# Kernel optimization log

Hardware: AMD Instinct MI355X
Metric: run time of the kernel (lower is better)

## Reference

```python
import jax, jax.numpy as jnp
import numpy as np

DIM_CAP = 16   # capsule dim
NCLS = 17      # annotation_nr
BS = 16
T = 120        # chunk_size * fps
P = 22         # players per frame graph
G = BS * T     # number of graphs = 1920
N = G * P      # nodes = 42240
C_IN = 14
CHS = [16, 32, 64, 152]  # 8m,16m,32m,76m with m=2
BN_EPS = 1e-3


def _build_graph():
    # fully-connected directed edges within each 22-node graph (no self loops)
    ii, jj = np.meshgrid(np.arange(P), np.arange(P), indexing='ij')
    mask = ii != jj
    li, lj = ii[mask], jj[mask]               # (462,)
    base = (np.arange(G) * P)[:, None]
    src = (base + li[None, :]).reshape(-1)
    dst = (base + lj[None, :]).reshape(-1)
    edge_index = np.stack([src, dst]).astype(np.int64)   # (2, E)
    batch = np.repeat(np.arange(G), P).astype(np.int64)  # (N,)
    return jnp.asarray(edge_index), jnp.asarray(batch)


def setup_inputs() -> dict:
    key = jax.random.key(0)
    ks = jax.random.split(key, 16)
    edge_index, batch = _build_graph()
    E = edge_index.shape[1]
    x = jax.random.normal(ks[0], (N, C_IN), dtype=jnp.float32)
    edge_attr = jax.random.uniform(ks[1], (E, 5), dtype=jnp.float32)
    dims = [C_IN] + CHS
    params = {}
    for i in range(4):
        s = 1.0 / np.sqrt(dims[i])
        params[f'W{i+1}'] = jax.random.normal(ks[2 + i], (dims[i], dims[i + 1]), dtype=jnp.float32) * s
        params[f'b{i+1}'] = jnp.zeros((dims[i + 1],), dtype=jnp.float32)
    c_out = DIM_CAP * NCLS  # 272
    params['conv_w'] = jax.random.normal(ks[6], (c_out, CHS[-1], 3), dtype=jnp.float32) * (1.0 / np.sqrt(CHS[-1] * 3))
    params['conv_b'] = jnp.zeros((c_out,), dtype=jnp.float32)
    params['bn_gamma'] = jnp.ones((T,), dtype=jnp.float32)
    params['bn_beta'] = jnp.zeros((T,), dtype=jnp.float32)
    return dict(x=x, edge_index=edge_index, batch=batch, edge_attr=edge_attr, **params)


def _gcn_layer(x, src, dst, w_edge, W, b):
    # PyG GCNConv: x' = D^-1/2 (A + I) D^-1/2 (x W) + b, edge weights w, self-loop weight 1
    n = x.shape[0]
    h = x @ W
    loop = jnp.arange(n)
    src_f = jnp.concatenate([src, loop])
    dst_f = jnp.concatenate([dst, loop])
    w_f = jnp.concatenate([w_edge, jnp.ones((n,), h.dtype)])
    deg = jax.ops.segment_sum(w_f, dst_f, num_segments=n)
    dinv = jnp.where(deg > 0, jax.lax.rsqrt(deg), 0.0)
    norm = dinv[src_f] * w_f * dinv[dst_f]
    out = jax.ops.segment_sum(norm[:, None] * h[src_f], dst_f, num_segments=n)
    return out + b


def reference(x, edge_index, batch, edge_attr, W1, b1, W2, b2, W3, b3, W4, b4,
              conv_w, conv_b, bn_gamma, bn_beta):
    src, dst = edge_index[0], edge_index[1]
    ew = edge_attr[:, 4]
    h = jax.nn.relu(_gcn_layer(x, src, dst, ew, W1, b1))
    h = jax.nn.relu(_gcn_layer(h, src, dst, ew, W2, b2))
    h = jax.nn.relu(_gcn_layer(h, src, dst, ew, W3, b3))
    h = jax.nn.relu(_gcn_layer(h, src, dst, ew, W4, b4))
    # global mean pool per graph -> (G, 152)
    ones = jnp.ones((h.shape[0],), h.dtype)
    cnt = jax.ops.segment_sum(ones, batch, num_segments=G)
    pooled = jax.ops.segment_sum(h, batch, num_segments=G) / jnp.clip(cnt, 1.0)[:, None]
    # (BS, T, 152) -> (BS, 152, T); conv kernel (3,1) with pad (1,1) on T
    feat = pooled.reshape(BS, T, CHS[-1]).transpose(0, 2, 1)
    conv = jax.lax.conv_general_dilated(
        feat, conv_w, window_strides=(1,), padding=[(1, 1)],
        dimension_numbers=('NCH', 'OIH', 'NCH'))
    conv = conv + conv_b[None, :, None]            # (BS, 272, T)
    caps = conv.transpose(0, 2, 1).reshape(BS, T, DIM_CAP, NCLS)
    # BatchNorm2d(num_features=T) in eval mode: running mean 0, var 1
    scale = (bn_gamma / jnp.sqrt(1.0 + BN_EPS))[None, :, None, None]
    shift = bn_beta[None, :, None, None]
    s = jax.nn.sigmoid(caps * scale + shift)
    out = jnp.sqrt(jnp.sum(jnp.square(s - 0.5), axis=2) * 4.0 / DIM_CAP)
    return out  # (BS, T, NCLS)
```

## Files before the change

### kernel.cpp

```cpp
#include <hip/hip_runtime.h>

#define GROUPS 1920
#define CH4 152

__device__ __forceinline__ int rh(int r) { return (r + (r >> 3)) & 7; }
__device__ __forceinline__ int swz(int r, int c) {
    return (r << 5) + ((((c >> 2) ^ rh(r)) << 2) | (c & 3));
}
__device__ __forceinline__ int swz4(int r, int c4) {
    return (r << 5) + ((c4 ^ rh(r)) << 2);
}

template<int DIN, int KR>
__device__ __forceinline__ void layerA(const float* buf, float* Ut,
                                       const float* A, int tid)
{
    constexpr int NT = (DIN / KR) * 3;
    if (tid < NT) {
        const int kt = tid / 3, pt = tid - kt * 3;
        const int p0 = pt * 8;
        float acc[KR][8];
        #pragma unroll
        for (int j = 0; j < KR; ++j)
            #pragma unroll
            for (int a = 0; a < 8; ++a) acc[j][a] = 0.f;
        #pragma unroll 2
        for (int q = 0; q < 22; ++q) {
            const float4 a0 = *(const float4*)(A + q * 28 + p0);
            const float4 a1 = *(const float4*)(A + q * 28 + p0 + 4);
            float xv[KR];
            #pragma unroll
            for (int j = 0; j < KR; ++j) xv[j] = buf[swz(kt * KR + j, q)];
            #pragma unroll
            for (int j = 0; j < KR; ++j) {
                acc[j][0] = fmaf(xv[j], a0.x, acc[j][0]);
                acc[j][1] = fmaf(xv[j], a0.y, acc[j][1]);
                acc[j][2] = fmaf(xv[j], a0.z, acc[j][2]);
                acc[j][3] = fmaf(xv[j], a0.w, acc[j][3]);
                acc[j][4] = fmaf(xv[j], a1.x, acc[j][4]);
                acc[j][5] = fmaf(xv[j], a1.y, acc[j][5]);
                acc[j][6] = fmaf(xv[j], a1.z, acc[j][6]);
                acc[j][7] = fmaf(xv[j], a1.w, acc[j][7]);
            }
        }
        #pragma unroll
        for (int j = 0; j < KR; ++j) {
            const int k = kt * KR + j;
            *(float4*)(Ut + swz4(k, pt * 2)) =
                make_float4(acc[j][0], acc[j][1], acc[j][2], acc[j][3]);
            *(float4*)(Ut + swz4(k, pt * 2 + 1)) =
                make_float4(acc[j][4], acc[j][5], acc[j][6], acc[j][7]);
        }
    }
}

template<int DIN, int DOUT, int CR>
__device__ __forceinline__ void layerB(const float* __restrict__ W,
                                       const float* __restrict__ Bb,
                                       const float* Ut, float* buf, int tid)
{
    constexpr int NT = (DOUT / CR) * 3;
    if (tid < NT) {
        const int ct = tid / 3, pt = tid - ct * 3;
        const int c0 = ct * CR;
        float acc[CR][8];
        #pragma unroll
        for (int b = 0; b < CR; ++b) {
            const float bias = Bb[c0 + b];
            #pragma unroll
            for (int a = 0; a < 8; ++a) acc[b][a] = bias;
        }
        #pragma unroll 4
        for (int k = 0; k < DIN; ++k) {
            const float4 u0 = *(const float4*)(Ut + swz4(k, pt * 2));
            const float4 u1 = *(const float4*)(Ut + swz4(k, pt * 2 + 1));
            float wv[CR];
            if constexpr (CR == 1) {
                wv[0] = W[k * DOUT + c0];
            } else if constexpr (CR == 2) {
                const float2 w2 = *(const float2*)(W + k * DOUT + c0);
                wv[0] = w2.x; wv[1] = w2.y;
            } else {
                #pragma unroll
                for (int b = 0; b < CR; b += 4) {
                    const float4 w4 = *(const float4*)(W + k * DOUT + c0 + b);
                    wv[b] = w4.x; wv[b + 1] = w4.y; wv[b + 2] = w4.z; wv[b + 3] = w4.w;
                }
            }
            #pragma unroll
            for (int b = 0; b < CR; ++b) {
                acc[b][0] = fmaf(wv[b], u0.x, acc[b][0]);
                acc[b][1] = fmaf(wv[b], u0.y, acc[b][1]);
                acc[b][2] = fmaf(wv[b], u0.z, acc[b][2]);
                acc[b][3] = fmaf(wv[b], u0.w, acc[b][3]);
                acc[b][4] = fmaf(wv[b], u1.x, acc[b][4]);
                acc[b][5] = fmaf(wv[b], u1.y, acc[b][5]);
                acc[b][6] = fmaf(wv[b], u1.z, acc[b][6]);
                acc[b][7] = fmaf(wv[b], u1.w, acc[b][7]);
            }
        }
        #pragma unroll
        for (int b = 0; b < CR; ++b) {
            const int r = c0 + b;
            *(float4*)(buf + swz4(r, pt * 2)) =
                make_float4(fmaxf(acc[b][0], 0.f), fmaxf(acc[b][1], 0.f),
                            fmaxf(acc[b][2], 0.f), fmaxf(acc[b][3], 0.f));
            *(float4*)(buf + swz4(r, pt * 2 + 1)) =
                make_float4(fmaxf(acc[b][4], 0.f), fmaxf(acc[b][5], 0.f),
                            fmaxf(acc[b][6], 0.f), fmaxf(acc[b][7], 0.f));
        }
    }
}

__global__ __launch_bounds__(128, 4) void gcn_kernel(
    const float* __restrict__ x, const float* __restrict__ ea,
    const float* __restrict__ W1, const float* __restrict__ b1,
    const float* __restrict__ W2, const float* __restrict__ b2,
    const float* __restrict__ W3, const float* __restrict__ b3,
    const float* __restrict__ W4, const float* __restrict__ b4,
    const float* __restrict__ cw, float* __restrict__ wT,
    float* __restrict__ pooled)
{
    __shared__ __align__(16) float sA[24 * 28];
    __shared__ float dv[24];
    __shared__ __align__(16) float buf[64 * 32];
    __shared__ __align__(16) float Ut[64 * 32];

    const int tid = threadIdx.x;
    const int g = blockIdx.x;
    const int b = g / 120, t = g - b * 120;

    {
        const int idx = g * 128 + tid;
        if (idx < 272 * 456) {
            const int o = idx / 456, r = idx - o * 456;
            wT[r * 272 + o] = cw[idx];
        }
    }
    if (t == 0 && tid < 152)   pooled[((size_t)(b * 122) + 0)   * 152 + tid] = 0.f;
    if (t == 119 && tid < 152) pooled[((size_t)(b * 122) + 121) * 152 + tid] = 0.f;

    for (int idx = tid; idx < 24 * 28; idx += 128) {
        const int q = idx / 28, p = idx - q * 28;
        float v = 0.f;
        if (q < 22 && p < 22) {
            if (q == p) v = 1.0f;
            else {
                const int e = q * 21 + p - (p > q);
                v = ea[((size_t)g * 462 + e) * 5 + 4];
            }
        }
        sA[idx] = v;
    }
    for (int idx = tid; idx < 14 * 24; idx += 128) {
        const int k = idx / 24, p = idx - k * 24;
        buf[swz(k, p)] = (p < 22) ? x[((size_t)g * 22 + p) * 14 + k] : 0.f;
    }
    __syncthreads();

    if (tid < 24) {
        const int p = tid;
        float s = 0.f;
        #pragma unroll
        for (int q = 0; q < 22; ++q) s += sA[q * 28 + p];
        dv[p] = (s > 0.f) ? rsqrtf(s) : 0.f;
    }
    __syncthreads();
    for (int idx = tid; idx < 24 * 28; idx += 128) {
        const int q = idx / 28, p = idx - q * 28;
        if (p < 24) sA[idx] *= dv[q] * dv[p];
    }
    __syncthreads();

    layerA<14, 1>(buf, Ut, sA, tid);           __syncthreads();
    layerB<14, 16, 1>(W1, b1, Ut, buf, tid);   __syncthreads();
    layerA<16, 1>(buf, Ut, sA, tid);           __syncthreads();
    layerB<16, 32, 1>(W2, b2, Ut, buf, tid);   __syncthreads();
    layerA<32, 1>(buf, Ut, sA, tid);           __syncthreads();
    layerB<32, 64, 2>(W3, b3, Ut, buf, tid);   __syncthreads();
    layerA<64, 2>(buf, Ut, sA, tid);           __syncthreads();

    float* pscr = sA;
    if (tid < 38 * 3) {
        const int ct = tid / 3, pt = tid - ct * 3;
        const int c0 = ct * 4;
        float acc[4][8];
        #pragma unroll
        for (int bb = 0; bb < 4; ++bb) {
            const float bias = b4[c0 + bb];
            #pragma unroll
            for (int a = 0; a < 8; ++a) acc[bb][a] = bias;
        }
        #pragma unroll 4
        for (int k = 0; k < 64; ++k) {
            const float4 u0 = *(const float4*)(Ut + swz4(k, pt * 2));
            const float4 u1 = *(const float4*)(Ut + swz4(k, pt * 2 + 1));
            const float4 w4 = *(const float4*)(W4 + k * 152 + c0);
            const float wv[4] = {w4.x, w4.y, w4.z, w4.w};
            #pragma unroll
            for (int bb = 0; bb < 4; ++bb) {
                acc[bb][0] = fmaf(wv[bb], u0.x, acc[bb][0]);
                acc[bb][1] = fmaf(wv[bb], u0.y, acc[bb][1]);
                acc[bb][2] = fmaf(wv[bb], u0.z, acc[bb][2]);
                acc[bb][3] = fmaf(wv[bb], u0.w, acc[bb][3]);
                acc[bb][4] = fmaf(wv[bb], u1.x, acc[bb][4]);
                acc[bb][5] = fmaf(wv[bb], u1.y, acc[bb][5]);
                acc[bb][6] = fmaf(wv[bb], u1.z, acc[bb][6]);
                acc[bb][7] = fmaf(wv[bb], u1.w, acc[bb][7]);
            }
        }
        const int alim = (pt == 2) ? 6 : 8;
        float ps[4];
        #pragma unroll
        for (int bb = 0; bb < 4; ++bb) {
            float s = 0.f;
            #pragma unroll
            for (int a = 0; a < 8; ++a)
                s += (a < alim) ? fmaxf(acc[bb][a], 0.f) : 0.f;
            ps[bb] = s;
        }
        *(float4*)(pscr + pt * 152 + c0) = make_float4(ps[0], ps[1], ps[2], ps[3]);
    }
    __syncthreads();

    {
        float* dst = pooled + ((size_t)(b * 122) + t + 1) * 152;
        for (int c = tid; c < 152; c += 128) {
            const float s = pscr[c] + pscr[152 + c] + pscr[304 + c];
            dst[c] = s * (1.0f / 22.0f);
        }
    }
}

__global__ __launch_bounds__(640) void conv_caps_kernel(
    const float* __restrict__ pG, const float* __restrict__ wT,
    const float* __restrict__ cb, const float* __restrict__ gamma,
    const float* __restrict__ beta, float* __restrict__ out)
{
    __shared__ __align__(16) float s2[4 * 272];
    __shared__ float sc[4], sh[4];

    const int bx = blockIdx.x;
    const int b = bx / 30, tile = bx - b * 30;
    const int t0 = tile * 4;
    const int tid = threadIdx.x;
    const int half = tid / 320;
    const int o = tid - half * 320;

    if (tid < 4) {
        sc[tid] = gamma[t0 + tid] * 0.999500374688f;
        sh[tid] = beta[t0 + tid];
    }

    float acc[4];
    if (o < 272) {
        const float a0 = half ? 0.f : cb[o];
        acc[0] = a0; acc[1] = a0; acc[2] = a0; acc[3] = a0;
        const int i0 = half * 76;
        const float* wp = wT + (size_t)i0 * 816 + o;
        const float* f  = pG + ((size_t)b * 122 + t0) * 152 + i0;
        #pragma unroll 2
        for (int i = 0; i < 76; ++i) {
            const float w0 = wp[0], w1 = wp[272], w2 = wp[544];
            float fr[6];
            #pragma unroll
            for (int j = 0; j < 6; ++j) fr[j] = f[j * 152];
            #pragma unroll
            for (int tt = 0; tt < 4; ++tt)
                acc[tt] = fmaf(w0, fr[tt], fmaf(w1, fr[tt + 1], fmaf(w2, fr[tt + 2], acc[tt])));
            wp += 816; f += 1;
        }
    }
    if (half == 1 && o < 272) {
        #pragma unroll
        for (int tt = 0; tt < 4; ++tt) s2[tt * 272 + o] = acc[tt];
    }
    __syncthreads();
    if (half == 0 && o < 272) {
        #pragma unroll
        for (int tt = 0; tt < 4; ++tt) {
            const float z = fmaf(acc[tt] + s2[tt * 272 + o], sc[tt], sh[tt]);
            const float s = 1.0f / (1.0f + __expf(-z));
            const float d = s - 0.5f;
            s2[tt * 272 + o] = d * d;
        }
    }
    __syncthreads();

    if (tid < 4 * 17) {
        const int tt = tid / 17, n = tid - tt * 17;
        float s = 0.f;
        #pragma unroll
        for (int d = 0; d < 16; ++d) s += s2[tt * 272 + d * 17 + n];
        out[((size_t)b * 120 + t0 + tt) * 17 + n] = sqrtf(s) * 0.5f;
    }
}

extern "C" void kernel_launch(void* const* d_in, const int* in_sizes, int n_in,
                              void* d_out, int out_size, void* d_ws, size_t ws_size,
                              hipStream_t stream) {
    const float* x     = (const float*)d_in[0];
    const float* ea    = (const float*)d_in[3];
    const float* W1    = (const float*)d_in[4];
    const float* b1    = (const float*)d_in[5];
    const float* W2    = (const float*)d_in[6];
    const float* b2    = (const float*)d_in[7];
    const float* W3    = (const float*)d_in[8];
    const float* b3    = (const float*)d_in[9];
    const float* W4    = (const float*)d_in[10];
    const float* b4    = (const float*)d_in[11];
    const float* cw    = (const float*)d_in[12];
    const float* cb    = (const float*)d_in[13];
    const float* gamma = (const float*)d_in[14];
    const float* beta  = (const float*)d_in[15];
    float* out = (float*)d_out;

    float* pG = (float*)d_ws;
    float* wT = pG + (size_t)16 * 122 * 152;

    hipLaunchKernelGGL(gcn_kernel, dim3(GROUPS), dim3(128), 0, stream,
                       x, ea, W1, b1, W2, b2, W3, b3, W4, b4, cw, wT, pG);
    hipLaunchKernelGGL(conv_caps_kernel, dim3(16 * 30), dim3(640), 0, stream,
                       pG, wT, cb, gamma, beta, out);
}
```

Baseline: 173.7 us.

## Read conv weights in native layout and stage pooled features in shared memory

```diff
diff --git a/kernel.cpp b/kernel.cpp
--- a/kernel.cpp
+++ b/kernel.cpp
@@ -118,7 +118,6 @@
     const float* __restrict__ W2, const float* __restrict__ b2,
     const float* __restrict__ W3, const float* __restrict__ b3,
     const float* __restrict__ W4, const float* __restrict__ b4,
-    const float* __restrict__ cw, float* __restrict__ wT,
     float* __restrict__ pooled)
 {
     __shared__ __align__(16) float sA[24 * 28];
@@ -130,13 +129,6 @@
     const int g = blockIdx.x;
     const int b = g / 120, t = g - b * 120;
 
-    {
-        const int idx = g * 128 + tid;
-        if (idx < 272 * 456) {
-            const int o = idx / 456, r = idx - o * 456;
-            wT[r * 272 + o] = cw[idx];
-        }
-    }
     if (t == 0 && tid < 152)   pooled[((size_t)(b * 122) + 0)   * 152 + tid] = 0.f;
     if (t == 119 && tid < 152) pooled[((size_t)(b * 122) + 121) * 152 + tid] = 0.f;
 
@@ -232,11 +224,12 @@
     }
 }
 
-__global__ __launch_bounds__(640) void conv_caps_kernel(
-    const float* __restrict__ pG, const float* __restrict__ wT,
+__global__ __launch_bounds__(320) void conv_caps_kernel(
+    const float* __restrict__ pG, const float* __restrict__ cw,
     const float* __restrict__ cb, const float* __restrict__ gamma,
     const float* __restrict__ beta, float* __restrict__ out)
 {
+    __shared__ __align__(16) float sf[6 * 160];
     __shared__ __align__(16) float s2[4 * 272];
     __shared__ float sc[4], sh[4];
 
@@ -244,42 +237,57 @@
     const int b = bx / 30, tile = bx - b * 30;
     const int t0 = tile * 4;
     const int tid = threadIdx.x;
-    const int half = tid / 320;
-    const int o = tid - half * 320;
 
     if (tid < 4) {
         sc[tid] = gamma[t0 + tid] * 0.999500374688f;
         sh[tid] = beta[t0 + tid];
     }
-
-    float acc[4];
-    if (o < 272) {
-        const float a0 = half ? 0.f : cb[o];
-        acc[0] = a0; acc[1] = a0; acc[2] = a0; acc[3] = a0;
-        const int i0 = half * 76;
-        const float* wp = wT + (size_t)i0 * 816 + o;
-        const float* f  = pG + ((size_t)b * 122 + t0) * 152 + i0;
+    {
+        const int r0 = b * 122 + t0;
+        const float* src = pG + (size_t)r0 * 152;
+        for (int idx = tid; idx < 6 * 152; idx += 320) {
+            const int row = idx / 152, c = idx - row * 152;
+            sf[row * 160 + c] = src[idx];
+        }
+    }
+    __syncthreads();
+
+    if (tid < 272) {
+        const int o = tid;
+        float acc[4];
+        {
+            const float a0 = cb[o];
+            acc[0] = a0; acc[1] = a0; acc[2] = a0; acc[3] = a0;
+        }
+        const float4* wp = (const float4*)(cw + (size_t)o * 456);
         #pragma unroll 2
-        for (int i = 0; i < 76; ++i) {
-            const float w0 = wp[0], w1 = wp[272], w2 = wp[544];
-            float fr[6];
-            #pragma unroll
-            for (int j = 0; j < 6; ++j) fr[j] = f[j * 152];
-            #pragma unroll
-            for (int tt = 0; tt < 4; ++tt)
-                acc[tt] = fmaf(w0, fr[tt], fmaf(w1, fr[tt + 1], fmaf(w2, fr[tt + 2], acc[tt])));
-            wp += 816; f += 1;
-        }
-    }
-    if (half == 1 && o < 272) {
-        #pragma unroll
-        for (int tt = 0; tt < 4; ++tt) s2[tt * 272 + o] = acc[tt];
-    }
-    __syncthreads();
-    if (half == 0 && o < 272) {
+        for (int ib = 0; ib < 38; ++ib) {
+            const float4 wa = wp[0], wb = wp[1], wc = wp[2];
+            wp += 3;
+            float w[12];
+            w[0] = wa.x; w[1] = wa.y; w[2]  = wa.z; w[3]  = wa.w;
+            w[4] = wb.x; w[5] = wb.y; w[6]  = wb.z; w[7]  = wb.w;
+            w[8] = wc.x; w[9] = wc.y; w[10] = wc.z; w[11] = wc.w;
+            float4 f4[6];
+            #pragma unroll
+            for (int j = 0; j < 6; ++j)
+                f4[j] = *(const float4*)(sf + j * 160 + ib * 4);
+            #pragma unroll
+            for (int u = 0; u < 4; ++u) {
+                #pragma unroll
+                for (int tt = 0; tt < 4; ++tt) {
+                    const float fa = ((const float*)&f4[tt])[u];
+                    const float fb = ((const float*)&f4[tt + 1])[u];
+                    const float fc = ((const float*)&f4[tt + 2])[u];
+                    acc[tt] = fmaf(w[u * 3 + 0], fa,
+                              fmaf(w[u * 3 + 1], fb,
+                              fmaf(w[u * 3 + 2], fc, acc[tt])));
+                }
+            }
+        }
         #pragma unroll
         for (int tt = 0; tt < 4; ++tt) {
-            const float z = fmaf(acc[tt] + s2[tt * 272 + o], sc[tt], sh[tt]);
+            const float z = fmaf(acc[tt], sc[tt], sh[tt]);
             const float s = 1.0f / (1.0f + __expf(-z));
             const float d = s - 0.5f;
             s2[tt * 272 + o] = d * d;
@@ -316,10 +324,9 @@
     float* out = (float*)d_out;
 
     float* pG = (float*)d_ws;
-    float* wT = pG + (size_t)16 * 122 * 152;
 
     hipLaunchKernelGGL(gcn_kernel, dim3(GROUPS), dim3(128), 0, stream,
-                       x, ea, W1, b1, W2, b2, W3, b3, W4, b4, cw, wT, pG);
-    hipLaunchKernelGGL(conv_caps_kernel, dim3(16 * 30), dim3(640), 0, stream,
-                       pG, wT, cb, gamma, beta, out);
-}
+                       x, ea, W1, b1, W2, b2, W3, b3, W4, b4, pG);
+    hipLaunchKernelGGL(conv_caps_kernel, dim3(16 * 30), dim3(320), 0, stream,
+                       pG, cw, cb, gamma, beta, out);
+}
```

After: 158.8 us. -8.5%, faster.

## Store pooled features time-major and restructure conv-caps to map time onto lanes

Applied to the files above, without the earlier changes.

```diff
diff --git a/kernel.cpp b/kernel.cpp
--- a/kernel.cpp
+++ b/kernel.cpp
@@ -118,8 +118,7 @@
     const float* __restrict__ W2, const float* __restrict__ b2,
     const float* __restrict__ W3, const float* __restrict__ b3,
     const float* __restrict__ W4, const float* __restrict__ b4,
-    const float* __restrict__ cw, float* __restrict__ wT,
-    float* __restrict__ pooled)
+    float* __restrict__ pT)
 {
     __shared__ __align__(16) float sA[24 * 28];
     __shared__ float dv[24];
@@ -130,15 +129,12 @@
     const int g = blockIdx.x;
     const int b = g / 120, t = g - b * 120;
 
-    {
-        const int idx = g * 128 + tid;
-        if (idx < 272 * 456) {
-            const int o = idx / 456, r = idx - o * 456;
-            wT[r * 272 + o] = cw[idx];
-        }
-    }
-    if (t == 0 && tid < 152)   pooled[((size_t)(b * 122) + 0)   * 152 + tid] = 0.f;
-    if (t == 119 && tid < 152) pooled[((size_t)(b * 122) + 121) * 152 + tid] = 0.f;
+    if (t == 0)
+        for (int j = tid; j < 152 * 4; j += 128)
+            pT[(((size_t)(b * 152) + (j >> 2)) << 7) + (j & 3)] = 0.f;
+    if (t == 119)
+        for (int j = tid; j < 152 * 4; j += 128)
+            pT[(((size_t)(b * 152) + (j >> 2)) << 7) + 124 + (j & 3)] = 0.f;
 
     for (int idx = tid; idx < 24 * 28; idx += 128) {
         const int q = idx / 28, p = idx - q * 28;
@@ -224,75 +220,66 @@
     __syncthreads();
 
     {
-        float* dst = pooled + ((size_t)(b * 122) + t + 1) * 152;
+        float* basep = pT + (((size_t)(b * 152)) << 7) + 4 + t;
         for (int c = tid; c < 152; c += 128) {
             const float s = pscr[c] + pscr[152 + c] + pscr[304 + c];
-            dst[c] = s * (1.0f / 22.0f);
-        }
-    }
-}
-
-__global__ __launch_bounds__(640) void conv_caps_kernel(
-    const float* __restrict__ pG, const float* __restrict__ wT,
+            basep[(size_t)c << 7] = s * (1.0f / 22.0f);
+        }
+    }
+}
+
+__global__ __launch_bounds__(256) void conv_caps_kernel(
+    const float* __restrict__ pT, const float* __restrict__ cw,
     const float* __restrict__ cb, const float* __restrict__ gamma,
     const float* __restrict__ beta, float* __restrict__ out)
 {
-    __shared__ __align__(16) float s2[4 * 272];
-    __shared__ float sc[4], sh[4];
+    __shared__ float sp[4 * 64];
 
     const int bx = blockIdx.x;
-    const int b = bx / 30, tile = bx - b * 30;
-    const int t0 = tile * 4;
+    const int b = bx / 34, r = bx - b * 34;
+    const int n = r >> 1, thalf = r & 1;
     const int tid = threadIdx.x;
-    const int half = tid / 320;
-    const int o = tid - half * 320;
-
-    if (tid < 4) {
-        sc[tid] = gamma[t0 + tid] * 0.999500374688f;
-        sh[tid] = beta[t0 + tid];
-    }
-
-    float acc[4];
-    if (o < 272) {
-        const float a0 = half ? 0.f : cb[o];
-        acc[0] = a0; acc[1] = a0; acc[2] = a0; acc[3] = a0;
-        const int i0 = half * 76;
-        const float* wp = wT + (size_t)i0 * 816 + o;
-        const float* f  = pG + ((size_t)b * 122 + t0) * 152 + i0;
-        #pragma unroll 2
-        for (int i = 0; i < 76; ++i) {
-            const float w0 = wp[0], w1 = wp[272], w2 = wp[544];
-            float fr[6];
-            #pragma unroll
-            for (int j = 0; j < 6; ++j) fr[j] = f[j * 152];
-            #pragma unroll
-            for (int tt = 0; tt < 4; ++tt)
-                acc[tt] = fmaf(w0, fr[tt], fmaf(w1, fr[tt + 1], fmaf(w2, fr[tt + 2], acc[tt])));
-            wp += 816; f += 1;
-        }
-    }
-    if (half == 1 && o < 272) {
-        #pragma unroll
-        for (int tt = 0; tt < 4; ++tt) s2[tt * 272 + o] = acc[tt];
-    }
-    __syncthreads();
-    if (half == 0 && o < 272) {
-        #pragma unroll
-        for (int tt = 0; tt < 4; ++tt) {
-            const float z = fmaf(acc[tt] + s2[tt * 272 + o], sc[tt], sh[tt]);
-            const float s = 1.0f / (1.0f + __expf(-z));
-            const float d = s - 0.5f;
-            s2[tt * 272 + o] = d * d;
-        }
-    }
-    __syncthreads();
-
-    if (tid < 4 * 17) {
-        const int tt = tid / 17, n = tid - tt * 17;
-        float s = 0.f;
-        #pragma unroll
-        for (int d = 0; d < 16; ++d) s += s2[tt * 272 + d * 17 + n];
-        out[((size_t)b * 120 + t0 + tt) * 17 + n] = sqrtf(s) * 0.5f;
+    const int wq = tid >> 6, lane = tid & 63;
+    const bool act = (lane < 60);
+    const int t = act ? (thalf * 60 + lane) : 119;
+
+    const float sct = gamma[t] * 0.999500374688f;
+    const float sht = beta[t];
+
+    const int o0 = wq * 68 + n;
+    float a0 = cb[o0], a1 = cb[o0 + 17], a2 = cb[o0 + 34], a3 = cb[o0 + 51];
+
+    const float* pf  = pT + (((size_t)b * 152) << 7) + 3 + t;
+    const float* wp0 = cw + (size_t)o0 * 456;
+    const float* wp1 = wp0 + 17 * 456;
+    const float* wp2 = wp0 + 34 * 456;
+    const float* wp3 = wp0 + 51 * 456;
+
+    #pragma unroll 4
+    for (int i = 0; i < 152; ++i) {
+        const float* fi = pf + ((size_t)i << 7);
+        const float f0 = fi[0], f1 = fi[1], f2 = fi[2];
+        const int iw = i * 3;
+        a0 = fmaf(wp0[iw], f0, fmaf(wp0[iw + 1], f1, fmaf(wp0[iw + 2], f2, a0)));
+        a1 = fmaf(wp1[iw], f0, fmaf(wp1[iw + 1], f1, fmaf(wp1[iw + 2], f2, a1)));
+        a2 = fmaf(wp2[iw], f0, fmaf(wp2[iw + 1], f1, fmaf(wp2[iw + 2], f2, a2)));
+        a3 = fmaf(wp3[iw], f0, fmaf(wp3[iw + 1], f1, fmaf(wp3[iw + 2], f2, a3)));
+    }
+
+    float sl;
+    {
+        float z, s, d;
+        z = fmaf(a0, sct, sht); s = 1.0f / (1.0f + __expf(-z)); d = s - 0.5f; sl  = d * d;
+        z = fmaf(a1, sct, sht); s = 1.0f / (1.0f + __expf(-z)); d = s - 0.5f; sl += d * d;
+        z = fmaf(a2, sct, sht); s = 1.0f / (1.0f + __expf(-z)); d = s - 0.5f; sl += d * d;
+        z = fmaf(a3, sct, sht); s = 1.0f / (1.0f + __expf(-z)); d = s - 0.5f; sl += d * d;
+    }
+    sp[wq * 64 + lane] = sl;
+    __syncthreads();
+
+    if (wq == 0 && act) {
+        const float s = sp[lane] + sp[64 + lane] + sp[128 + lane] + sp[192 + lane];
+        out[((size_t)b * 120 + t) * 17 + n] = sqrtf(s) * 0.5f;
     }
 }
 
@@ -315,11 +302,10 @@
     const float* beta  = (const float*)d_in[15];
     float* out = (float*)d_out;
 
-    float* pG = (float*)d_ws;
-    float* wT = pG + (size_t)16 * 122 * 152;
+    float* pT = (float*)d_ws;
 
     hipLaunchKernelGGL(gcn_kernel, dim3(GROUPS), dim3(128), 0, stream,
-                       x, ea, W1, b1, W2, b2, W3, b3, W4, b4, cw, wT, pG);
-    hipLaunchKernelGGL(conv_caps_kernel, dim3(16 * 30), dim3(640), 0, stream,
-                       pG, wT, cb, gamma, beta, out);
-}
+                       x, ea, W1, b1, W2, b2, W3, b3, W4, b4, pT);
+    hipLaunchKernelGGL(conv_caps_kernel, dim3(16 * 34), dim3(256), 0, stream,
+                       pT, cw, cb, gamma, beta, out);
+}
```

Measured after the change: 182.7 us. +5.2%, slower.
